# Optimization experiments

Hardware: AMD Instinct MI355X
Metric: run time of the kernel (lower is better)

Reference implementation:

```python
import jax, jax.numpy as jnp
import numpy as np

NUM_HEADS = 12
EMBED_DIM = 768
HEAD_DIM = EMBED_DIM // NUM_HEADS


def setup_inputs() -> dict:
    key = jax.random.key(0)
    ks = jax.random.split(key, 9)
    B, S, D = 8, 1025, EMBED_DIM
    s = 1.0 / np.sqrt(D)
    return {
        "x": jax.random.normal(ks[0], (B, S, D), dtype=jnp.float32),
        "Wk": jax.random.normal(ks[1], (D, D), dtype=jnp.float32) * s,
        "bk": jnp.zeros((D,), dtype=jnp.float32),
        "Wq": jax.random.normal(ks[2], (D, D), dtype=jnp.float32) * s,
        "bq": jnp.zeros((D,), dtype=jnp.float32),
        "Wv": jax.random.normal(ks[3], (D, D), dtype=jnp.float32) * s,
        "bv": jnp.zeros((D,), dtype=jnp.float32),
        "Wp": jax.random.normal(ks[4], (D, D), dtype=jnp.float32) * s,
        "bp": jnp.zeros((D,), dtype=jnp.float32),
    }


def reference(x, Wk, bk, Wq, bq, Wv, bv, Wp, bp):
    B, S, D = x.shape
    H, Hd = NUM_HEADS, HEAD_DIM
    # Linear projections (torch Linear: y = x @ W^T + b)
    k = (x @ Wk.T + bk).reshape(B, S, H, Hd).transpose(0, 2, 1, 3)  # (B,H,S,Hd)
    q = (x @ Wq.T + bq).reshape(B, S, H, Hd).transpose(0, 2, 1, 3)
    v = (x @ Wv.T + bv).reshape(B, S, H, Hd).transpose(0, 2, 1, 3)
    scale = 1.0 / jnp.sqrt(jnp.asarray(Hd, dtype=x.dtype))
    scores = jnp.einsum("bhqd,bhkd->bhqk", q, k) * scale  # (B,H,S,S)
    attn = jax.nn.softmax(scores, axis=-1)
    # dropout is identity at inference (eval mode)
    out = jnp.einsum("bhqk,bhkd->bhqd", attn, v)  # (B,H,S,Hd)
    out = out.transpose(0, 2, 1, 3).reshape(B, S, D)
    return out @ Wp.T + bp
```

## Files before the change

kernel.cpp:

```cpp
#include <hip/hip_runtime.h>
#include <stdint.h>

#define BATCH  8
#define SEQ    1025
#define DMODEL 768
#define NHEAD  12
#define HDIM   64
#define MTOT   (BATCH * SEQ)
#define MPAD   8320
#define SPAD   1056
#define BHTOT  (BATCH * NHEAD)
#define QT32   33
#define NTILE  17
#define NKSTEP 12
#define QKSCALE 0.18033688011112042f

typedef __bf16 bf16x8 __attribute__((ext_vector_type(8)));
typedef __bf16 bf16x4 __attribute__((ext_vector_type(4)));
typedef float  f32x4  __attribute__((ext_vector_type(4)));
typedef float  f32x16 __attribute__((ext_vector_type(16)));

#if __has_builtin(__builtin_amdgcn_exp2f)
#define EXP2F __builtin_amdgcn_exp2f
#else
#define EXP2F exp2f
#endif

constexpr size_t XB_OFF  = 0;
constexpr size_t XB_SZ   = (size_t)MPAD * DMODEL * 2;
constexpr size_t W_SZ    = (size_t)DMODEL * DMODEL * 2;
constexpr size_t WQB_OFF = XB_OFF + XB_SZ;
constexpr size_t WKB_OFF = WQB_OFF + W_SZ;
constexpr size_t WVB_OFF = WKB_OFF + W_SZ;
constexpr size_t WPB_OFF = WVB_OFF + W_SZ;
constexpr size_t QB_OFF  = WPB_OFF + W_SZ;
constexpr size_t QB_SZ   = (size_t)BHTOT * SEQ * HDIM * 2;
constexpr size_t KB_OFF  = QB_OFF + QB_SZ;
constexpr size_t VT_OFF  = KB_OFF + QB_SZ;
constexpr size_t VT_SZ   = (size_t)BHTOT * HDIM * SPAD * 2;
constexpr size_t AO_OFF  = XB_OFF;
constexpr size_t WS_NEEDED = VT_OFF + VT_SZ;

__device__ __forceinline__ void async16(const void* g, void* l) {
  __builtin_amdgcn_global_load_lds((__attribute__((address_space(1))) void*)g,
                                   (__attribute__((address_space(3))) void*)l,
                                   16, 0, 0);
}

__device__ __forceinline__ unsigned pkbf(float lo, float hi) {
  __bf16 l = (__bf16)lo, h = (__bf16)hi;
  unsigned short lb = __builtin_bit_cast(unsigned short, l);
  unsigned short hb = __builtin_bit_cast(unsigned short, h);
  return ((unsigned)hb << 16) | (unsigned)lb;
}
__device__ __forceinline__ unsigned shfl32u(unsigned x) {
  return (unsigned)__shfl_xor((int)x, 32, 64);
}
__device__ __forceinline__ float pairmax(float x) {
  return fmaxf(x, __shfl_xor(x, 32, 64));
}
__device__ __forceinline__ float pairsum(float x) {
  return x + __shfl_xor(x, 32, 64);
}

__device__ __forceinline__ float tree_max16(const f32x16& s) {
  float a0 = fmaxf(s[0], s[1]),   a1 = fmaxf(s[2], s[3]);
  float a2 = fmaxf(s[4], s[5]),   a3 = fmaxf(s[6], s[7]);
  float a4 = fmaxf(s[8], s[9]),   a5 = fmaxf(s[10], s[11]);
  float a6 = fmaxf(s[12], s[13]), a7 = fmaxf(s[14], s[15]);
  float b0 = fmaxf(a0, a1), b1 = fmaxf(a2, a3);
  float b2 = fmaxf(a4, a5), b3 = fmaxf(a6, a7);
  return fmaxf(fmaxf(b0, b1), fmaxf(b2, b3));
}
__device__ __forceinline__ float tree_sum16(const f32x16& s) {
  float a0 = s[0] + s[1],   a1 = s[2] + s[3];
  float a2 = s[4] + s[5],   a3 = s[6] + s[7];
  float a4 = s[8] + s[9],   a5 = s[10] + s[11];
  float a6 = s[12] + s[13], a7 = s[14] + s[15];
  float b0 = a0 + a1, b1 = a2 + a3, b2 = a4 + a5, b3 = a6 + a7;
  return (b0 + b1) + (b2 + b3);
}

#define XCONV_BLKS 6240
#define WCONV_BLKS 576

__global__ void __launch_bounds__(256)
convert_all(const float* __restrict__ x,
            const float* __restrict__ w0, const float* __restrict__ w1,
            const float* __restrict__ w2, const float* __restrict__ w3,
            __bf16* __restrict__ xb, __bf16* __restrict__ wdst) {
  int b = blockIdx.x;
  if (b < XCONV_BLKS) {
    const int n_src = MTOT * DMODEL;
    int idx = (b * 256 + threadIdx.x) * 4;
    bf16x4 o;
    if (idx + 3 < n_src) {
      float4 v = *(const float4*)&x[idx];
      o[0] = (__bf16)v.x; o[1] = (__bf16)v.y; o[2] = (__bf16)v.z; o[3] = (__bf16)v.w;
    } else {
      #pragma unroll
      for (int t = 0; t < 4; ++t) {
        int k = idx + t;
        o[t] = (k < n_src) ? (__bf16)x[k] : (__bf16)0.f;
      }
    }
    *(bf16x4*)&xb[idx] = o;
  } else {
    b -= XCONV_BLKS;
    const int which = b / WCONV_BLKS;
    const int bb = b - which * WCONV_BLKS;
    const float* src = (which == 0) ? w0 : (which == 1) ? w1 : (which == 2) ? w2 : w3;
    __bf16* d = wdst + (size_t)which * DMODEL * DMODEL;
    const int idx = (bb * 256 + threadIdx.x) * 4;
    float4 v = *(const float4*)&src[idx];
    bf16x4 o;
    o[0] = (__bf16)v.x; o[1] = (__bf16)v.y; o[2] = (__bf16)v.z; o[3] = (__bf16)v.w;
    *(bf16x4*)&d[idx] = o;
  }
}

__device__ __forceinline__ void stage_step(const __bf16* const (&sa)[4],
                                           const __bf16* const (&sw)[4],
                                           __bf16* As, __bf16* Bs,
                                           int kt, int tid) {
  #pragma unroll
  for (int i = 0; i < 4; ++i) {
    const int gi = i * 256 + tid;
    async16(sa[i] + kt, As + gi * 8);
    async16(sw[i] + kt, Bs + gi * 8);
  }
}

__device__ __forceinline__ void compute_tile(const __bf16* __restrict__ pa,
                                             const __bf16* __restrict__ pb,
                                             int off0, int off1,
                                             f32x4 acc[4][4]) {
  #pragma unroll
  for (int kk = 0; kk < 2; ++kk) {
    const int offk = kk ? off1 : off0;
    bf16x8 af[4], bfr[4];
    #pragma unroll
    for (int i = 0; i < 4; ++i)
      af[i] = *(const bf16x8*)(pa + i * 1024 + offk);
    #pragma unroll
    for (int j = 0; j < 4; ++j)
      bfr[j] = *(const bf16x8*)(pb + j * 1024 + offk);
    __builtin_amdgcn_s_setprio(1);
    #pragma unroll
    for (int i = 0; i < 4; ++i)
      #pragma unroll
      for (int j = 0; j < 4; ++j)
        acc[i][j] = __builtin_amdgcn_mfma_f32_16x16x32_bf16(af[i], bfr[j], acc[i][j], 0, 0, 0);
    __builtin_amdgcn_s_setprio(0);
  }
}

#define GC_WAIT8  asm volatile("s_waitcnt vmcnt(8)" ::: "memory")
#define GC_WAIT0  asm volatile("s_waitcnt vmcnt(0)" ::: "memory")
#define GC_BAR    __builtin_amdgcn_s_barrier()
#define GC_SCHED  __builtin_amdgcn_sched_barrier(0)

__device__ __forceinline__ void gemm_core(const __bf16* __restrict__ A,
                                          const __bf16* __restrict__ W,
                                          __bf16 (*As)[128 * 64], __bf16 (*Bs)[128 * 64],
                                          int m0, int n0, f32x4 acc[4][4]) {
  const int tid  = threadIdx.x;
  const int lane = tid & 63;
  const int wave = tid >> 6;
  const int wm = wave >> 1, wn = wave & 1;
  const int l15 = lane & 15, lg = lane >> 4;
  const int rx  = l15 & 7;

  const __bf16* sa[4];
  const __bf16* sw[4];
  #pragma unroll
  for (int i = 0; i < 4; ++i) {
    const int gi = i * 256 + tid;
    const int r  = gi >> 3;
    const int g  = (gi & 7) ^ (r & 7);
    sa[i] = A + (size_t)(m0 + r) * DMODEL + g * 8;
    sw[i] = W + (size_t)(n0 + r) * DMODEL + g * 8;
  }
  const int off0 = ((0 * 4 + lg) ^ rx) * 8;
  const int off1 = ((1 * 4 + lg) ^ rx) * 8;
  const __bf16* paA0 = &As[0][(wm * 64 + l15) * 64];
  const __bf16* paA1 = &As[1][(wm * 64 + l15) * 64];
  const __bf16* pbB0 = &Bs[0][(wn * 64 + l15) * 64];
  const __bf16* pbB1 = &Bs[1][(wn * 64 + l15) * 64];

  stage_step(sa, sw, As[0], Bs[0], 0, tid);

  #pragma unroll 1
  for (int tt = 0; tt < NKSTEP / 2; ++tt) {
    const int t = tt * 2;
    stage_step(sa, sw, As[1], Bs[1], (t + 1) * 64, tid);
    GC_WAIT8;
    GC_BAR;
    GC_SCHED;
    compute_tile(paA0, pbB0, off0, off1, acc);
    GC_BAR;
    GC_SCHED;
    if (t + 2 < NKSTEP) {
      stage_step(sa, sw, As[0], Bs[0], (t + 2) * 64, tid);
      GC_WAIT8;
    } else {
      GC_WAIT0;
    }
    GC_BAR;
    GC_SCHED;
    compute_tile(paA1, pbB1, off0, off1, acc);
    GC_BAR;
    GC_SCHED;
  }
}

#define EPSW 136

__global__ void __launch_bounds__(256)
gemm_qkv_kernel(const __bf16* __restrict__ xb, const __bf16* __restrict__ wsb,
                const float* __restrict__ bq, const float* __restrict__ bk,
                const float* __restrict__ bv,
                __bf16* __restrict__ qb, __bf16* __restrict__ kb,
                __bf16* __restrict__ vtb) {
  __shared__ __attribute__((aligned(16))) char smem[65536];
  __bf16 (*As)[128 * 64] = (__bf16 (*)[128 * 64])smem;
  __bf16 (*Bs)[128 * 64] = (__bf16 (*)[128 * 64])(smem + 32768);

  const int wg  = blockIdx.x;
  const int xcd = wg & 7, idx = wg >> 3;
  const int v   = xcd * 146 + (xcd < 2 ? xcd : 2) + idx;
  const int m0  = (v / 18) * 128;
  const int n0  = (v % 18) * 128;

  f32x4 acc[4][4];
  #pragma unroll
  for (int i = 0; i < 4; ++i)
    #pragma unroll
    for (int j = 0; j < 4; ++j) acc[i][j] = (f32x4){0.f, 0.f, 0.f, 0.f};

  gemm_core(xb, wsb, As, Bs, m0, n0, acc);

  const int tid  = threadIdx.x;
  const int lane = tid & 63;
  const int wave = tid >> 6;
  const int wm = wave >> 1, wn = wave & 1;
  const int l15 = lane & 15, lg = lane >> 4;
  const int mode = n0 / 768;
  const int nmod = n0 - mode * 768;
  const float* bias = (mode == 0) ? bq : (mode == 1) ? bk : bv;
  const float scale = (mode == 0) ? QKSCALE : 1.f;
  __bf16* eps = (__bf16*)smem;

  #pragma unroll
  for (int i = 0; i < 4; ++i) {
    #pragma unroll
    for (int j = 0; j < 4; ++j) {
      const int ncol = wn * 64 + j * 16 + l15;
      const float bb = bias[nmod + ncol];
      #pragma unroll
      for (int r = 0; r < 4; ++r) {
        const int mrow = wm * 64 + i * 16 + lg * 4 + r;
        const __bf16 val = (__bf16)((acc[i][j][r] + bb) * scale);
        if (mode < 2) eps[mrow * EPSW + ncol] = val;
        else          eps[ncol * EPSW + mrow] = val;
      }
    }
  }
  __syncthreads();

  if (mode < 2) {
    __bf16* dst0 = (mode == 0) ? qb : kb;
    #pragma unroll
    for (int p = 0; p < 8; ++p) {
      const int g = p * 256 + tid;
      const int mrow = g >> 4, gc = g & 15;
      const int mg = m0 + mrow;
      if (mg < MTOT) {
        const int b = mg / SEQ;
        const int s = mg - b * SEQ;
        const int colbase = nmod + gc * 8;
        const int h = colbase >> 6, hd = colbase & 63;
        bf16x8 w = *(const bf16x8*)&eps[mrow * EPSW + gc * 8];
        *(bf16x8*)(dst0 + ((size_t)(b * NHEAD + h) * SEQ + s) * HDIM + hd) = w;
      }
    }
  } else {
    #pragma unroll
    for (int p = 0; p < 8; ++p) {
      const int g = p * 256 + tid;
      const int ncol = g >> 4, gc = g & 15;
      const int mr0 = gc * 8;
      const int colbase = nmod + ncol;
      const int h = colbase >> 6, hd = colbase & 63;
      #pragma unroll
      for (int u = 0; u < 8; ++u) {
        const int mg = m0 + mr0 + u;
        if (mg < MTOT) {
          const int b = mg / SEQ;
          const int s = mg - b * SEQ;
          vtb[((size_t)(b * NHEAD + h) * HDIM + hd) * SPAD + s] =
              eps[ncol * EPSW + mr0 + u];
        }
      }
    }
  }
}

__global__ void __launch_bounds__(256)
gemm_proj_kernel(const __bf16* __restrict__ ab, const __bf16* __restrict__ wpb,
                 const float* __restrict__ bp, float* __restrict__ out) {
  __shared__ __attribute__((aligned(16))) char smem[65536];
  __bf16 (*As)[128 * 64] = (__bf16 (*)[128 * 64])smem;
  __bf16 (*Bs)[128 * 64] = (__bf16 (*)[128 * 64])(smem + 32768);
  const int wg  = blockIdx.x;
  const int xcd = wg & 7, idx = wg >> 3;
  const int v   = xcd * 48 + (xcd < 6 ? xcd : 6) + idx;
  const int m0  = (v / 6) * 128;
  const int n0  = (v % 6) * 128;

  f32x4 acc[4][4];
  #pragma unroll
  for (int i = 0; i < 4; ++i)
    #pragma unroll
    for (int j = 0; j < 4; ++j) acc[i][j] = (f32x4){0.f, 0.f, 0.f, 0.f};

  gemm_core(ab, wpb, As, Bs, m0, n0, acc);

  const int lane = threadIdx.x & 63;
  const int wave = threadIdx.x >> 6;
  const int wm = wave >> 1, wn = wave & 1;
  const int l15 = lane & 15, lg = lane >> 4;
  #pragma unroll
  for (int i = 0; i < 4; ++i) {
    #pragma unroll
    for (int j = 0; j < 4; ++j) {
      const int ncol = n0 + wn * 64 + j * 16 + l15;
      const float bb = bp[ncol];
      #pragma unroll
      for (int r = 0; r < 4; ++r) {
        const int mrow = m0 + wm * 64 + i * 16 + lg * 4 + r;
        if (mrow < MTOT) out[(size_t)mrow * DMODEL + ncol] = acc[i][j][r] + bb;
      }
    }
  }
}

__device__ __forceinline__ void build_pa(const f32x16& s, int hi, bf16x8 pa[2]) {
  #pragma unroll
  for (int sl2 = 0; sl2 < 2; ++sl2) {
    const int off = sl2 * 8;
    unsigned w0 = pkbf(s[off + 0], s[off + 1]);
    unsigned w1 = pkbf(s[off + 2], s[off + 3]);
    unsigned w2 = pkbf(s[off + 4], s[off + 5]);
    unsigned w3 = pkbf(s[off + 6], s[off + 7]);
    unsigned p0 = shfl32u(w0), p1 = shfl32u(w1);
    unsigned p2 = shfl32u(w2), p3 = shfl32u(w3);
    unsigned pw[4];
    pw[0] = hi ? p2 : w0;
    pw[1] = hi ? p3 : w1;
    pw[2] = hi ? w2 : p0;
    pw[3] = hi ? w3 : p1;
    __builtin_memcpy(&pa[sl2], pw, 16);
  }
}

__device__ __forceinline__ void stage_kv(const __bf16* __restrict__ Kp,
                                         const __bf16* __restrict__ Vp,
                                         __bf16* kls, __bf16* vls,
                                         int k0, int tid) {
  const int r = tid >> 3, p = tid & 7;
  const int g = p ^ (r & 7);
  async16(Kp + (size_t)(k0 + r) * HDIM + g * 8, kls + tid * 8);
  int col = k0 + g * 8;
  if (col >= SPAD) col = 0;
  async16(Vp + (size_t)r * SPAD + col, vls + tid * 8);
}

template<bool MASK>
__device__ __forceinline__ void attn_tile64(const __bf16* __restrict__ kls,
                                            const __bf16* __restrict__ vls,
                                            const bf16x8 (&qf)[4], int l31, int hi,
                                            float& mrun, float& lrun,
                                            f32x16& o0, f32x16& o1) {
  f32x16 s0, s1;
  #pragma unroll
  for (int r = 0; r < 16; ++r) { s0[r] = 0.f; s1[r] = 0.f; }
  {
    const int kr0 = l31,      krx0 = kr0 & 7;
    const int kr1 = 32 + l31, krx1 = kr1 & 7;
    #pragma unroll
    for (int sl = 0; sl < 4; ++sl) {
      bf16x8 kf0 = *(const bf16x8*)&kls[(kr0 * 8 + ((2 * sl + hi) ^ krx0)) * 8];
      bf16x8 kf1 = *(const bf16x8*)&kls[(kr1 * 8 + ((2 * sl + hi) ^ krx1)) * 8];
      s0 = __builtin_amdgcn_mfma_f32_32x32x16_bf16(kf0, qf[sl], s0, 0, 0, 0);
      s1 = __builtin_amdgcn_mfma_f32_32x32x16_bf16(kf1, qf[sl], s1, 0, 0, 0);
    }
  }
  if (MASK) {
    #pragma unroll
    for (int r = 1; r < 16; ++r) s0[r] = -1e30f;
    if (hi) s0[0] = -1e30f;
    #pragma unroll
    for (int r = 0; r < 16; ++r) s1[r] = -1e30f;
  }

  const float mloc = pairmax(fmaxf(tree_max16(s0), tree_max16(s1)));
  if (!__all(mloc - mrun <= 8.f)) {
    const float mnew = fmaxf(mrun, mloc);
    const float corr = EXP2F(mrun - mnew);
    lrun *= corr;
    #pragma unroll
    for (int r = 0; r < 16; ++r) { o0[r] *= corr; o1[r] *= corr; }
    mrun = mnew;
  }
  #pragma unroll
  for (int r = 0; r < 16; ++r) { s0[r] = EXP2F(s0[r] - mrun); s1[r] = EXP2F(s1[r] - mrun); }
  lrun += pairsum(tree_sum16(s0) + tree_sum16(s1));

  bf16x8 pa0[2], pa1[2];
  build_pa(s0, hi, pa0);
  build_pa(s1, hi, pa1);

  #pragma unroll
  for (int ot = 0; ot < 2; ++ot) {
    const int vr = ot * 32 + l31;
    const int vrx = vr & 7;
    f32x16& o = ot ? o1 : o0;
    #pragma unroll
    for (int j = 0; j < 2; ++j) {
      bf16x8 vf0 = *(const bf16x8*)&vls[(vr * 8 + ((2 * j + hi) ^ vrx)) * 8];
      bf16x8 vf1 = *(const bf16x8*)&vls[(vr * 8 + ((4 + 2 * j + hi) ^ vrx)) * 8];
      o = __builtin_amdgcn_mfma_f32_32x32x16_bf16(vf0, pa0[j], o, 0, 0, 0);
      o = __builtin_amdgcn_mfma_f32_32x32x16_bf16(vf1, pa1[j], o, 0, 0, 0);
    }
  }
}

__global__ void __launch_bounds__(512, 4)
attn_kernel(const __bf16* __restrict__ qb, const __bf16* __restrict__ kb,
            const __bf16* __restrict__ vtb, __bf16* __restrict__ ao) {
  __shared__ __bf16 kls[2][64 * 64];
  __shared__ __bf16 vls[2][64 * 64];

  const int tid  = threadIdx.x;
  const int wid  = tid >> 6;
  const int lane = tid & 63;
  const int l31 = lane & 31, hi = (lane >> 5) & 1;

  const int bid = blockIdx.x;
  const int xcd = bid & 7;
  const int ixd = bid >> 3;
  const int bh  = xcd * (BHTOT / 8) + ixd / 5;
  const int qblk = ixd % 5;
  const int qt  = qblk * 8 + wid;
  const bool active = qt < QT32;

  const __bf16* Qp = qb + (size_t)bh * SEQ * HDIM;
  const __bf16* Kp = kb + (size_t)bh * SEQ * HDIM;
  const __bf16* Vp = vtb + (size_t)bh * HDIM * SPAD;

  const int qidx = qt * 32 + l31;
  const int qc = (qidx < SEQ ? qidx : SEQ - 1);
  bf16x8 qf[4];
  if (active) {
    #pragma unroll
    for (int sl = 0; sl < 4; ++sl)
      qf[sl] = *(const bf16x8*)&Qp[(size_t)qc * HDIM + sl * 16 + hi * 8];
  }

  f32x16 o0, o1;
  #pragma unroll
  for (int r = 0; r < 16; ++r) { o0[r] = 0.f; o1[r] = 0.f; }
  float mrun = -1e30f, lrun = 0.f;

  stage_kv(Kp, Vp, kls[0], vls[0], 0, tid);
  __syncthreads();

  for (int t = 0; t < NTILE; ++t) {
    const int cur = t & 1;
    if (t + 1 < NTILE)
      stage_kv(Kp, Vp, kls[cur ^ 1], vls[cur ^ 1], (t + 1) * 64, tid);
    if (active) {
      if (t < NTILE - 1)
        attn_tile64<false>(kls[cur], vls[cur], qf, l31, hi, mrun, lrun, o0, o1);
      else
        attn_tile64<true>(kls[cur], vls[cur], qf, l31, hi, mrun, lrun, o0, o1);
    }
    __syncthreads();
  }

  if (active && qidx < SEQ) {
    const int b = bh / NHEAD, h = bh % NHEAD;
    const float inv = 1.f / lrun;
    __bf16* base = ao + ((size_t)b * SEQ + qidx) * DMODEL + h * HDIM + hi * 4;
    #pragma unroll
    for (int t = 0; t < 2; ++t) {
      const f32x16& o = t ? o1 : o0;
      #pragma unroll
      for (int g = 0; g < 4; ++g) {
        bf16x4 w;
        #pragma unroll
        for (int u = 0; u < 4; ++u) w[u] = (__bf16)(o[g * 4 + u] * inv);
        *(bf16x4*)(base + t * 32 + g * 8) = w;
      }
    }
  }
}

extern "C" void kernel_launch(void* const* d_in, const int* in_sizes, int n_in,
                              void* d_out, int out_size, void* d_ws, size_t ws_size,
                              hipStream_t stream) {
  const float* x  = (const float*)d_in[0];
  const float* Wk = (const float*)d_in[1];
  const float* bk = (const float*)d_in[2];
  const float* Wq = (const float*)d_in[3];
  const float* bq = (const float*)d_in[4];
  const float* Wv = (const float*)d_in[5];
  const float* bv = (const float*)d_in[6];
  const float* Wp = (const float*)d_in[7];
  const float* bp = (const float*)d_in[8];
  float* out = (float*)d_out;

  if (ws_size < WS_NEEDED) return;

  char* ws = (char*)d_ws;
  __bf16* xb  = (__bf16*)(ws + XB_OFF);
  __bf16* wqb = (__bf16*)(ws + WQB_OFF);
  __bf16* wpb = (__bf16*)(ws + WPB_OFF);
  __bf16* qb  = (__bf16*)(ws + QB_OFF);
  __bf16* kb  = (__bf16*)(ws + KB_OFF);
  __bf16* vtb = (__bf16*)(ws + VT_OFF);
  __bf16* ab  = (__bf16*)(ws + AO_OFF);

  hipMemsetAsync(vtb, 0, VT_SZ, stream);

  convert_all<<<dim3(XCONV_BLKS + 4 * WCONV_BLKS), dim3(256), 0, stream>>>(
      x, Wq, Wk, Wv, Wp, xb, wqb);

  gemm_qkv_kernel<<<dim3(1170), dim3(256), 0, stream>>>(
      xb, wqb, bq, bk, bv, qb, kb, vtb);

  attn_kernel<<<dim3(8 * (BHTOT / 8) * 5), dim3(512), 0, stream>>>(qb, kb, vtb, ab);

  gemm_proj_kernel<<<dim3(390), dim3(256), 0, stream>>>(ab, wpb, bp, out);
}
```

Baseline: 150.4 us.

## Split KV tiles across wave pairs in attention and merge partial softmax states

Each 32-row query tile is now handled by a pair of waves, one taking even KV tiles and the other odd. The two partial results (running max, sum and output accumulators) are combined through shared memory at the end. The grid grows from 5 to 9 query blocks per head, giving more blocks and shorter per-wave serial chains. In exchange, every block still stages all K/V tiles, so K/V traffic per query roughly doubles, and the final merge adds an extra barrier plus shared-memory round trip.

```diff
diff --git a/kernel.cpp b/kernel.cpp
--- a/kernel.cpp
+++ b/kernel.cpp
@@ -439,20 +439,24 @@
 __global__ void __launch_bounds__(512, 4)
 attn_kernel(const __bf16* __restrict__ qb, const __bf16* __restrict__ kb,
             const __bf16* __restrict__ vtb, __bf16* __restrict__ ao) {
-  __shared__ __bf16 kls[2][64 * 64];
-  __shared__ __bf16 vls[2][64 * 64];
+  __shared__ __attribute__((aligned(16))) char smem[32768];
+  __bf16 (*kls)[64 * 64] = (__bf16 (*)[64 * 64])smem;
+  __bf16 (*vls)[64 * 64] = (__bf16 (*)[64 * 64])(smem + 16384);
+  __shared__ float mlbuf[4][2][64];
 
   const int tid  = threadIdx.x;
   const int wid  = tid >> 6;
   const int lane = tid & 63;
   const int l31 = lane & 31, hi = (lane >> 5) & 1;
+  const int pairid = wid >> 1;
+  const int ksplit = wid & 1;
 
   const int bid = blockIdx.x;
   const int xcd = bid & 7;
   const int ixd = bid >> 3;
-  const int bh  = xcd * (BHTOT / 8) + ixd / 5;
-  const int qblk = ixd % 5;
-  const int qt  = qblk * 8 + wid;
+  const int bh  = xcd * (BHTOT / 8) + ixd / 9;
+  const int qblk = ixd % 9;
+  const int qt  = qblk * 4 + pairid;
   const bool active = qt < QT32;
 
   const __bf16* Qp = qb + (size_t)bh * SEQ * HDIM;
@@ -480,7 +484,7 @@
     const int cur = t & 1;
     if (t + 1 < NTILE)
       stage_kv(Kp, Vp, kls[cur ^ 1], vls[cur ^ 1], (t + 1) * 64, tid);
-    if (active) {
+    if (active && (t & 1) == ksplit) {
       if (t < NTILE - 1)
         attn_tile64<false>(kls[cur], vls[cur], qf, l31, hi, mrun, lrun, o0, o1);
       else
@@ -489,9 +493,28 @@
     __syncthreads();
   }
 
-  if (active && qidx < SEQ) {
+  float* obuf = (float*)smem;
+  if (active && ksplit == 1) {
+    mlbuf[pairid][0][lane] = mrun;
+    mlbuf[pairid][1][lane] = lrun;
+    #pragma unroll
+    for (int r = 0; r < 16; ++r) {
+      obuf[(pairid * 32 + r) * 64 + lane]      = o0[r];
+      obuf[(pairid * 32 + 16 + r) * 64 + lane] = o1[r];
+    }
+  }
+  __syncthreads();
+  if (!active || ksplit == 1) return;
+
+  const float m1 = mlbuf[pairid][0][lane];
+  const float l1 = mlbuf[pairid][1][lane];
+  const float M  = fmaxf(mrun, m1);
+  const float c0 = EXP2F(mrun - M);
+  const float c1 = EXP2F(m1 - M);
+  const float inv = 1.f / (lrun * c0 + l1 * c1);
+
+  if (qidx < SEQ) {
     const int b = bh / NHEAD, h = bh % NHEAD;
-    const float inv = 1.f / lrun;
     __bf16* base = ao + ((size_t)b * SEQ + qidx) * DMODEL + h * HDIM + hi * 4;
     #pragma unroll
     for (int t = 0; t < 2; ++t) {
@@ -500,7 +523,11 @@
       for (int g = 0; g < 4; ++g) {
         bf16x4 w;
         #pragma unroll
-        for (int u = 0; u < 4; ++u) w[u] = (__bf16)(o[g * 4 + u] * inv);
+        for (int u = 0; u < 4; ++u) {
+          const int r = g * 4 + u;
+          const float part = obuf[(pairid * 32 + t * 16 + r) * 64 + lane];
+          w[u] = (__bf16)((o[r] * c0 + part * c1) * inv);
+        }
         *(bf16x4*)(base + t * 32 + g * 8) = w;
       }
     }
@@ -540,7 +567,7 @@
   gemm_qkv_kernel<<<dim3(1170), dim3(256), 0, stream>>>(
       xb, wqb, bq, bk, bv, qb, kb, vtb);
 
-  attn_kernel<<<dim3(8 * (BHTOT / 8) * 5), dim3(512), 0, stream>>>(qb, kb, vtb, ab);
+  attn_kernel<<<dim3(8 * (BHTOT / 8) * 9), dim3(512), 0, stream>>>(qb, kb, vtb, ab);
 
   gemm_proj_kernel<<<dim3(390), dim3(256), 0, stream>>>(ab, wpb, bp, out);
 }
```

New measurement: 169.2 us. +12.5%, slower.
